# Performance work log

Hardware: AMD Instinct MI355X
Metric: run time of the kernel (lower is better)

Reference implementation:

```python
import jax, jax.numpy as jnp
import numpy as np

NEG = jnp.float32(-1e30)  # finite stand-in for -inf (keeps vjp NaN-free)


def setup_inputs() -> dict:
    key = jax.random.key(0)
    k1, k2, k3 = jax.random.split(key, 3)
    B, T, C, L = 64, 128, 6625, 25
    predicts = jax.random.normal(k1, (B, T, C), dtype=jnp.float32)
    # blank=0, so valid label ids are 1..C-1
    labels = jax.random.randint(k2, (B, L), 1, C).astype(jnp.int64)
    label_lengths = jax.random.randint(k3, (B,), 1, L + 1).astype(jnp.int64)
    return {"predicts": predicts, "labels": labels, "label_lengths": label_lengths}


def _ctc_loss(log_probs, labels, label_lengths, blank=0):
    # log_probs: [T, B, C]; labels: [B, L]; label_lengths: [B]
    T, B, C = log_probs.shape
    L = labels.shape[1]
    S = 2 * L + 1
    # extended label sequence with interleaved blanks: [B, S]
    ext = jnp.full((B, S), blank, dtype=jnp.int32)
    ext = ext.at[:, 1::2].set(labels.astype(jnp.int32))
    # transition from s-2 allowed iff ext[s] != blank and ext[s] != ext[s-2]
    ext_sm2 = jnp.pad(ext[:, :-2], ((0, 0), (2, 0)), constant_values=blank)
    skip_ok = (ext != blank) & (ext != ext_sm2)  # [B, S]

    def lp_ext(lp_t):  # [B, C] -> [B, S], gather per-symbol log-probs
        return jnp.take_along_axis(lp_t, ext, axis=1)

    # alpha init at t=0
    lp0 = lp_ext(log_probs[0])
    alpha0 = jnp.full((B, S), NEG)
    alpha0 = alpha0.at[:, 0].set(lp0[:, 0])
    alpha0 = alpha0.at[:, 1].set(lp0[:, 1])

    def step(alpha, lp_t):
        a1 = jnp.pad(alpha[:, :-1], ((0, 0), (1, 0)), constant_values=NEG)
        a2 = jnp.pad(alpha[:, :-2], ((0, 0), (2, 0)), constant_values=NEG)
        a2 = jnp.where(skip_ok, a2, NEG)
        m = jnp.maximum(jnp.maximum(alpha, a1), a2)
        lse = m + jnp.log(jnp.exp(alpha - m) + jnp.exp(a1 - m) + jnp.exp(a2 - m))
        return lse + lp_ext(lp_t), None

    alphaT, _ = jax.lax.scan(step, alpha0, log_probs[1:])  # [B, S]

    # total log-likelihood ends at s = 2*len (blank) or s = 2*len - 1 (last label)
    idx_last = (2 * label_lengths).astype(jnp.int32)
    aL = jnp.take_along_axis(alphaT, idx_last[:, None], axis=1)[:, 0]
    aP = jnp.take_along_axis(alphaT, (idx_last - 1)[:, None], axis=1)[:, 0]
    m = jnp.maximum(aL, aP)
    loss = -(m + jnp.log(jnp.exp(aL - m) + jnp.exp(aP - m)))
    # zero_infinity=True
    loss = jnp.where(loss < 1e29, loss, 0.0)
    return loss  # [B]


def reference(predicts, labels, label_lengths):
    # predicts: [B, T, C] -> [T, B, C], then log_softmax over classes
    log_probs = jax.nn.log_softmax(jnp.transpose(predicts, (1, 0, 2)), axis=2)
    loss = _ctc_loss(log_probs, labels, label_lengths, blank=0)
    return jnp.mean(loss)
```

## Files before the change

### kernel.cpp

```cpp
#include <hip/hip_runtime.h>
#include <stdint.h>
#include <math.h>

constexpr int B = 64, T = 128, C = 6625, L = 25;
constexpr int S = 2 * L + 1;
constexpr int NCLS = L + 1;

#define LOG2E  1.44269504088896340736f
#define LN2    0.69314718055994530942f
#define NEG2   (-1.4426950408889634e30f)
#define NEGINF (-1e38f)

template <bool GATHER>
__global__ __launch_bounds__(256) void k_lse_gather(
    const float* __restrict__ predicts, const int* __restrict__ labels,
    float* __restrict__ lse_out, float* __restrict__ lp_out,
    float* __restrict__ out)
{
    const int row = blockIdx.x;
    const int b   = row >> 7;
    const int tid = threadIdx.x;
    const float* rp = predicts + (size_t)row * C;

    if (row == 0 && tid == 255) out[0] = 0.0f;

    const int mis  = (int)(((uintptr_t)rp >> 2) & 3);
    const int head = (4 - mis) & 3;
    const int nvec = (C - head) >> 2;
    const int tail = C - head - (nvec << 2);
    const float4* vp = (const float4*)(rp + head);

    float4 v[7];
#pragma unroll
    for (int j = 0; j < 7; ++j) {
        const int i = tid + j * 256;
        v[j] = (i < nvec) ? vp[i] : make_float4(NEGINF, NEGINF, NEGINF, NEGINF);
    }
    float sc = NEGINF;
    if (tid < head)                      sc = rp[tid];
    else if (tid >= 4 && tid < 4 + tail) sc = rp[head + (nvec << 2) + (tid - 4)];

    float s0 = __expf(sc), s1 = 0.0f, s2 = 0.0f, s3 = 0.0f;
#pragma unroll
    for (int j = 0; j < 7; ++j) {
        s0 += __expf(v[j].x); s1 += __expf(v[j].y);
        s2 += __expf(v[j].z); s3 += __expf(v[j].w);
    }
    float s = (s0 + s1) + (s2 + s3);

    const int wave = tid >> 6, lane = tid & 63;
    for (int off = 32; off; off >>= 1) s += __shfl_down(s, off);
    __shared__ float ssum[4];
    if (lane == 0) ssum[wave] = s;
    __syncthreads();
    const float lse = __logf((ssum[0] + ssum[1]) + (ssum[2] + ssum[3]));

    if (GATHER) {
        if (tid < NCLS) {
            const int cls = (tid == 0) ? 0 : labels[b * L + tid - 1];
            lp_out[(size_t)row * NCLS + tid] = (rp[cls] - lse) * LOG2E;
        }
    } else {
        if (tid == 0) lse_out[row] = lse;
    }
}

template <bool USE_LP>
__global__ __launch_bounds__(64) void k_ctc(
    const float* __restrict__ predicts, const int* __restrict__ labels,
    const int* __restrict__ lens, const float* __restrict__ lse,
    const float* __restrict__ lp_ws, float* __restrict__ out)
{
    const int b = blockIdx.x;
    const int s = threadIdx.x;
    const int  li = s >> 1;
    const bool isLab = (s & 1) && (s < S);

    const int myLab = isLab ? labels[b * L + li] : 0;
    const bool allow_skip = isLab && (s >= 3) && (myLab != labels[b * L + li - 1]);
    const int  k   = isLab ? (1 + li) : 0;
    const int  cls = isLab ? myLab : 0;

    auto fetch = [&](int t) -> float {
        const int row = b * T + t;
        if (USE_LP) return lp_ws[(size_t)row * NCLS + k];
        else        return (predicts[(size_t)row * C + cls] - lse[row]) * LOG2E;
    };
    auto step = [&](float& alpha, float lp2) {
        float a1 = __shfl_up(alpha, 1);
        float a2 = __shfl_up(alpha, 2);
        if (s < 1) a1 = NEG2;
        if (!allow_skip) a2 = NEG2;
        const float mm  = fmaxf(alpha, fmaxf(a1, a2));
        const float sum = exp2f(alpha - mm) + exp2f(a1 - mm) + exp2f(a2 - mm);
        alpha = mm + log2f(sum) + lp2;
    };

    constexpr int CH = 16;
    float Av[CH], Bv[CH];
#pragma unroll
    for (int i = 0; i < CH; ++i) Av[i] = fetch(i);
    float alpha = (s <= 1) ? Av[0] : NEG2;

#pragma unroll
    for (int t0 = 0; t0 < T; t0 += 2 * CH) {
#pragma unroll
        for (int i = 0; i < CH; ++i) { const int tt = t0 + CH + i;     Bv[i] = (tt < T) ? fetch(tt) : 0.0f; }
#pragma unroll
        for (int i = 0; i < CH; ++i) { if (t0 == 0 && i == 0) continue; step(alpha, Av[i]); }
#pragma unroll
        for (int i = 0; i < CH; ++i) { const int tt = t0 + 2 * CH + i; Av[i] = (tt < T) ? fetch(tt) : 0.0f; }
#pragma unroll
        for (int i = 0; i < CH; ++i) step(alpha, Bv[i]);
    }

    const int len = lens[b];
    const int idx = 2 * len;
    const float aL = __shfl(alpha, idx);
    const float aP = __shfl(alpha, idx - 1);
    if (s == 0) {
        const float mm = fmaxf(aL, aP);
        float loss = -(mm + log2f(exp2f(aL - mm) + exp2f(aP - mm))) * LN2;
        if (!(loss < 1e29f)) loss = 0.0f;
        atomicAdd(out, loss * (1.0f / (float)B));
    }
}

extern "C" void kernel_launch(void* const* d_in, const int* in_sizes, int n_in,
                              void* d_out, int out_size, void* d_ws, size_t ws_size,
                              hipStream_t stream)
{
    const float* predicts = (const float*)d_in[0];
    const int*   labels   = (const int*)d_in[1];
    const int*   lens     = (const int*)d_in[2];
    float*       out      = (float*)d_out;

    char* ws = (char*)d_ws;
    const size_t lp_bytes = (size_t)B * T * NCLS * sizeof(float);

    if (ws_size >= lp_bytes) {
        float* lp_ws = (float*)ws;
        k_lse_gather<true><<<B * T, 256, 0, stream>>>(predicts, labels, nullptr, lp_ws, out);
        k_ctc<true><<<B, 64, 0, stream>>>(predicts, labels, lens, nullptr, lp_ws, out);
    } else {
        float* lse_ws = (float*)ws;
        k_lse_gather<false><<<B * T, 256, 0, stream>>>(predicts, labels, lse_ws, nullptr, out);
        k_ctc<false><<<B, 64, 0, stream>>>(predicts, labels, lens, lse_ws, nullptr, out);
    }
}
```

Before: 54.88 us.

## Split row sum-exp across two blocks and gather label log-probs in CTC kernel

The first kernel now launches two blocks per (b,t) row, each summing exp over half of the classes and writing a partial sum, which doubles block-level parallelism and cuts per-thread registers. The per-row label gather and log-prob workspace are removed. The CTC kernel instead combines the two partials, takes log2, and reads the label logit directly from predicts. This trades a smaller workspace and a shorter first kernel for scattered global reads of predicts and extra log2 work inside the serial CTC kernel. A simpler fallback path is also added for small workspaces.

```diff
diff --git a/kernel.cpp b/kernel.cpp
--- a/kernel.cpp
+++ b/kernel.cpp
@@ -4,72 +4,61 @@
 
 constexpr int B = 64, T = 128, C = 6625, L = 25;
 constexpr int S = 2 * L + 1;
-constexpr int NCLS = L + 1;
+constexpr int HALF0 = 3312;
 
 #define LOG2E  1.44269504088896340736f
 #define LN2    0.69314718055994530942f
 #define NEG2   (-1.4426950408889634e30f)
 #define NEGINF (-1e38f)
 
-template <bool GATHER>
-__global__ __launch_bounds__(256) void k_lse_gather(
-    const float* __restrict__ predicts, const int* __restrict__ labels,
-    float* __restrict__ lse_out, float* __restrict__ lp_out,
+__global__ __launch_bounds__(256) void k_partial(
+    const float* __restrict__ predicts, float* __restrict__ part,
     float* __restrict__ out)
 {
-    const int row = blockIdx.x;
-    const int b   = row >> 7;
+    const int bid = blockIdx.x;
+    const int row = bid >> 1, h = bid & 1;
+    const int start = h ? HALF0 : 0;
+    const int len   = h ? (C - HALF0) : HALF0;
     const int tid = threadIdx.x;
-    const float* rp = predicts + (size_t)row * C;
+    const float* bp = predicts + (size_t)row * C + start;
 
-    if (row == 0 && tid == 255) out[0] = 0.0f;
+    if (bid == 0 && tid == 255) out[0] = 0.0f;
 
-    const int mis  = (int)(((uintptr_t)rp >> 2) & 3);
+    const int mis  = (int)(((uintptr_t)bp >> 2) & 3);
     const int head = (4 - mis) & 3;
-    const int nvec = (C - head) >> 2;
-    const int tail = C - head - (nvec << 2);
-    const float4* vp = (const float4*)(rp + head);
+    const int nvec = (len - head) >> 2;
+    const int tail = len - head - (nvec << 2);
+    const float4* vp = (const float4*)(bp + head);
 
-    float4 v[7];
+    float4 v[4];
 #pragma unroll
-    for (int j = 0; j < 7; ++j) {
+    for (int j = 0; j < 4; ++j) {
         const int i = tid + j * 256;
         v[j] = (i < nvec) ? vp[i] : make_float4(NEGINF, NEGINF, NEGINF, NEGINF);
     }
     float sc = NEGINF;
-    if (tid < head)                      sc = rp[tid];
-    else if (tid >= 4 && tid < 4 + tail) sc = rp[head + (nvec << 2) + (tid - 4)];
+    if (tid < head)                      sc = bp[tid];
+    else if (tid >= 4 && tid < 4 + tail) sc = bp[head + (nvec << 2) + (tid - 4)];
 
     float s0 = __expf(sc), s1 = 0.0f, s2 = 0.0f, s3 = 0.0f;
 #pragma unroll
-    for (int j = 0; j < 7; ++j) {
+    for (int j = 0; j < 4; ++j) {
         s0 += __expf(v[j].x); s1 += __expf(v[j].y);
         s2 += __expf(v[j].z); s3 += __expf(v[j].w);
     }
     float s = (s0 + s1) + (s2 + s3);
 
-    const int wave = tid >> 6, lane = tid & 63;
     for (int off = 32; off; off >>= 1) s += __shfl_down(s, off);
     __shared__ float ssum[4];
-    if (lane == 0) ssum[wave] = s;
+    if ((tid & 63) == 0) ssum[tid >> 6] = s;
     __syncthreads();
-    const float lse = __logf((ssum[0] + ssum[1]) + (ssum[2] + ssum[3]));
-
-    if (GATHER) {
-        if (tid < NCLS) {
-            const int cls = (tid == 0) ? 0 : labels[b * L + tid - 1];
-            lp_out[(size_t)row * NCLS + tid] = (rp[cls] - lse) * LOG2E;
-        }
-    } else {
-        if (tid == 0) lse_out[row] = lse;
-    }
+    if (tid == 0) part[bid] = (ssum[0] + ssum[1]) + (ssum[2] + ssum[3]);
 }
 
-template <bool USE_LP>
 __global__ __launch_bounds__(64) void k_ctc(
     const float* __restrict__ predicts, const int* __restrict__ labels,
-    const int* __restrict__ lens, const float* __restrict__ lse,
-    const float* __restrict__ lp_ws, float* __restrict__ out)
+    const int* __restrict__ lens, const float* __restrict__ part,
+    float* __restrict__ out)
 {
     const int b = blockIdx.x;
     const int s = threadIdx.x;
@@ -78,13 +67,13 @@
 
     const int myLab = isLab ? labels[b * L + li] : 0;
     const bool allow_skip = isLab && (s >= 3) && (myLab != labels[b * L + li - 1]);
-    const int  k   = isLab ? (1 + li) : 0;
     const int  cls = isLab ? myLab : 0;
 
     auto fetch = [&](int t) -> float {
         const int row = b * T + t;
-        if (USE_LP) return lp_ws[(size_t)row * NCLS + k];
-        else        return (predicts[(size_t)row * C + cls] - lse[row]) * LOG2E;
+        const float p = part[2 * row] + part[2 * row + 1];
+        const float x = predicts[(size_t)row * C + cls];
+        return fmaf(x, LOG2E, -log2f(p));
     };
     auto step = [&](float& alpha, float lp2) {
         float a1 = __shfl_up(alpha, 1);
@@ -126,6 +115,63 @@
     }
 }
 
+__global__ __launch_bounds__(256) void k_lse_only(
+    const float* __restrict__ predicts, float* __restrict__ lse_out,
+    float* __restrict__ out)
+{
+    const int row = blockIdx.x;
+    const int tid = threadIdx.x;
+    const float* rp = predicts + (size_t)row * C;
+    if (row == 0 && tid == 255) out[0] = 0.0f;
+
+    float s = 0.0f;
+    for (int c = tid; c < C; c += 256) s += __expf(rp[c]);
+    for (int off = 32; off; off >>= 1) s += __shfl_down(s, off);
+    __shared__ float ssum[4];
+    if ((tid & 63) == 0) ssum[tid >> 6] = s;
+    __syncthreads();
+    if (tid == 0) lse_out[row] = __logf((ssum[0] + ssum[1]) + (ssum[2] + ssum[3]));
+}
+
+__global__ __launch_bounds__(64) void k_ctc_slow(
+    const float* __restrict__ predicts, const int* __restrict__ labels,
+    const int* __restrict__ lens, const float* __restrict__ lse,
+    float* __restrict__ out)
+{
+    const int b = blockIdx.x;
+    const int s = threadIdx.x;
+    const int li = s >> 1;
+    const bool isLab = (s & 1) && (s < S);
+    const int myLab = isLab ? labels[b * L + li] : 0;
+    const bool allow_skip = isLab && (s >= 3) && (myLab != labels[b * L + li - 1]);
+    const int cls = isLab ? myLab : 0;
+
+    auto fetch = [&](int t) -> float {
+        const int row = b * T + t;
+        return (predicts[(size_t)row * C + cls] - lse[row]) * LOG2E;
+    };
+    float alpha = (s <= 1) ? fetch(0) : NEG2;
+    for (int t = 1; t < T; ++t) {
+        const float lpt = fetch(t);
+        float a1 = __shfl_up(alpha, 1);
+        float a2 = __shfl_up(alpha, 2);
+        if (s < 1) a1 = NEG2;
+        if (!allow_skip) a2 = NEG2;
+        const float mm  = fmaxf(alpha, fmaxf(a1, a2));
+        alpha = mm + log2f(exp2f(alpha - mm) + exp2f(a1 - mm) + exp2f(a2 - mm)) + lpt;
+    }
+    const int len = lens[b];
+    const int idx = 2 * len;
+    const float aL = __shfl(alpha, idx);
+    const float aP = __shfl(alpha, idx - 1);
+    if (s == 0) {
+        const float mm = fmaxf(aL, aP);
+        float loss = -(mm + log2f(exp2f(aL - mm) + exp2f(aP - mm))) * LN2;
+        if (!(loss < 1e29f)) loss = 0.0f;
+        atomicAdd(out, loss * (1.0f / (float)B));
+    }
+}
+
 extern "C" void kernel_launch(void* const* d_in, const int* in_sizes, int n_in,
                               void* d_out, int out_size, void* d_ws, size_t ws_size,
                               hipStream_t stream)
@@ -136,15 +182,15 @@
     float*       out      = (float*)d_out;
 
     char* ws = (char*)d_ws;
-    const size_t lp_bytes = (size_t)B * T * NCLS * sizeof(float);
+    const size_t part_bytes = (size_t)B * T * 2 * sizeof(float);
 
-    if (ws_size >= lp_bytes) {
-        float* lp_ws = (float*)ws;
-        k_lse_gather<true><<<B * T, 256, 0, stream>>>(predicts, labels, nullptr, lp_ws, out);
-        k_ctc<true><<<B, 64, 0, stream>>>(predicts, labels, lens, nullptr, lp_ws, out);
+    if (ws_size >= part_bytes) {
+        float* part = (float*)ws;
+        k_partial<<<B * T * 2, 256, 0, stream>>>(predicts, part, out);
+        k_ctc<<<B, 64, 0, stream>>>(predicts, labels, lens, part, out);
     } else {
         float* lse_ws = (float*)ws;
-        k_lse_gather<false><<<B * T, 256, 0, stream>>>(predicts, labels, lse_ws, nullptr, out);
-        k_ctc<false><<<B, 64, 0, stream>>>(predicts, labels, lens, lse_ws, nullptr, out);
+        k_lse_only<<<B * T, 256, 0, stream>>>(predicts, lse_ws, out);
+        k_ctc_slow<<<B, 64, 0, stream>>>(predicts, labels, lens, lse_ws, out);
     }
 }
```

Measured after the change: 62.17 us. 13.3% more time.
